# Optimization experiments

Measured on AMD Instinct MI355X. Metric: run time of the kernel, lower is better.

## Reference

```python
import jax, jax.numpy as jnp
import numpy as np

B, C, H, W = 8, 256, 128, 128
HEADS = 8


def setup_inputs() -> dict:
    key = jax.random.key(0)
    ks = jax.random.split(key, 9)
    d = {"x": jax.random.normal(ks[0], (B, C, H, W), jnp.float32)}
    for i, name in enumerate(["q", "k", "v", "o"]):
        # 1x1 conv == dense over channel dim; weight [C_out, C_in]
        d["W" + name] = jax.random.normal(ks[1 + 2 * i], (C, C), jnp.float32) * (C ** -0.5)
        d["b" + name] = jax.random.normal(ks[2 + 2 * i], (C,), jnp.float32) * 0.01
    return d


def reference(x, Wq, bq, Wk, bk, Wv, bv, Wo, bo):
    b, c, h, w = x.shape
    heads = HEADS
    hd = c // heads
    scale = hd ** -0.5

    def proj(Wm, bm):
        y = jnp.einsum('bchw,oc->bohw', x, Wm) + bm[None, :, None, None]
        return y.reshape(b, heads, hd, h, w)

    q = proj(Wq, bq)
    k = proj(Wk, bk)
    v = proj(Wv, bv)

    # horizontal attention: per row y, attention over width positions (w x v)
    attn_h = jax.nn.softmax(jnp.einsum('bhdyw,bhdyv->bhywv', q, k) * scale, axis=-1)
    out_h = jnp.einsum('bhywv,bhdyv->bhdyw', attn_h, v)

    # vertical attention: per column w, attention over height positions (y x z)
    attn_w = jax.nn.softmax(jnp.einsum('bhdyw,bhdzw->bhwyz', q, k) * scale, axis=-1)
    out_w = jnp.einsum('bhwyz,bhdzw->bhdyw', attn_w, v)

    out = (out_h + out_w).reshape(b, c, h, w)
    out = jnp.einsum('bchw,oc->bohw', out, Wo) + bo[None, :, None, None]
    return out + x
```

## Files before the change

### kernel.cpp

```cpp
#include <hip/hip_runtime.h>

#define B_ 8
#define C_ 256
#define HH 128
#define WW 128
#define HEADS_ 8
#define SCALE 0.17677669529663687f

typedef short v8s __attribute__((ext_vector_type(8)));
typedef float f32x4 __attribute__((ext_vector_type(4)));

__device__ __forceinline__ unsigned short f2bf(float f){
  unsigned int u = __float_as_uint(f);
  u += 0x7FFFu + ((u>>16)&1u);
  return (unsigned short)(u>>16);
}
__device__ __forceinline__ float bf2f(unsigned short s){ return __uint_as_float(((unsigned int)s)<<16); }
__device__ __forceinline__ f32x4 mfma16(v8s a, v8s b, f32x4 c){
  return __builtin_amdgcn_mfma_f32_16x16x32_bf16(a,b,c,0,0,0);
}
__device__ __forceinline__ int xs_idx(int s,int c){ return s*256 + ((((c>>3)^(s&31))&31)<<3) + (c&7); }
__device__ __forceinline__ int wl_idx(int dm,int c){ return dm*256 + ((((c>>3)^(dm&31))&31)<<3) + (c&7); }
__device__ __forceinline__ void gload_lds16(const void* g, void* l){
  __builtin_amdgcn_global_load_lds((const __attribute__((address_space(1))) unsigned int*)g,
                                   (__attribute__((address_space(3))) unsigned int*)l, 16, 0, 0);
}

#define WS_NEED1 201850880ULL
#define WS_NEED2 268959744ULL

__global__ __launch_bounds__(512,4)
void prep_w_kernel(const float* __restrict__ Wq, const float* __restrict__ Wk,
                   const float* __restrict__ Wv, const float* __restrict__ Wo,
                   unsigned short* __restrict__ wsW, unsigned short* __restrict__ wsWo){
  const int bid = blockIdx.x, t = threadIdx.x;
  if (bid < 96){
    int h = bid/12, seg = bid%12;
    int dm = seg*8 + (t>>6), c = (t&63)*4;
    const float* Wm = dm<32 ? Wq : (dm<64 ? Wk : Wv);
    const float4 w4 = *(const float4*)&Wm[(h*32 + (dm&31))*C_ + c];
    ushort4 pk = { f2bf(w4.x), f2bf(w4.y), f2bf(w4.z), f2bf(w4.w) };
    *(ushort4*)(wsW + h*24576 + wl_idx(dm, c)) = pk;
  } else {
    int q = bid - 96;
    int oc = q>>2, seg = q&3;
    int o = seg*8 + (t>>6), c = (t&63)*4;
    const float4 w4 = *(const float4*)&Wo[(oc*32+o)*C_ + c];
    ushort4 pk = { f2bf(w4.x), f2bf(w4.y), f2bf(w4.z), f2bf(w4.w) };
    *(ushort4*)(wsWo + oc*8192 + wl_idx(o, c)) = pk;
  }
}

__global__ __launch_bounds__(512,2)
void proj_kernel(const float* __restrict__ x,
                 const float* __restrict__ bq, const float* __restrict__ bk,
                 const float* __restrict__ bv,
                 const unsigned short* __restrict__ wsW,
                 unsigned short* __restrict__ Qw, unsigned short* __restrict__ Kw,
                 unsigned short* __restrict__ Vw){
  __shared__ __align__(16) char smem[141696];
  unsigned short* xs = (unsigned short*)smem;
  unsigned short* wl = (unsigned short*)(smem + 65536);
  unsigned short* rp = (unsigned short*)(smem + 114688);
  float* biasl       = (float*)(smem + 141312);

  const int tid = threadIdx.x;
  const int b = blockIdx.x >> 7, pt = blockIdx.x & 127;
  const size_t pos0 = (size_t)pt * 128;

  {
    const int cq = (tid>>5)*2, pl = (tid&31)*4;
    #pragma unroll
    for (int j=0;j<8;++j){
      int c0 = j*32 + cq;
      const float4 a0 = *(const float4*)&x[((size_t)(b*C_ + c0  ))*16384 + pos0 + pl];
      const float4 a1 = *(const float4*)&x[((size_t)(b*C_ + c0+1))*16384 + pos0 + pl];
      unsigned int p0 = (unsigned)f2bf(a0.x) | ((unsigned)f2bf(a1.x)<<16);
      unsigned int p1 = (unsigned)f2bf(a0.y) | ((unsigned)f2bf(a1.y)<<16);
      unsigned int p2 = (unsigned)f2bf(a0.z) | ((unsigned)f2bf(a1.z)<<16);
      unsigned int p3 = (unsigned)f2bf(a0.w) | ((unsigned)f2bf(a1.w)<<16);
      *(unsigned int*)&xs[xs_idx(pl+0, c0)] = p0;
      *(unsigned int*)&xs[xs_idx(pl+1, c0)] = p1;
      *(unsigned int*)&xs[xs_idx(pl+2, c0)] = p2;
      *(unsigned int*)&xs[xs_idx(pl+3, c0)] = p3;
    }
  }
  {
    const char* wb = (const char*)wsW;
    for (int rIt=0;rIt<6;++rIt)
      gload_lds16(wb + (rIt*512+tid)*16, (char*)wl + (rIt*512+tid)*16);
  }

  const int lane = tid&63, wv = tid>>6, lr = lane&15, lk = lane>>4;
  const f32x4 zero4 = {0.f,0.f,0.f,0.f};

  for (int h=0; h<HEADS_; ++h){
    __syncthreads();
    if (tid<96){
      int mat = tid>>5;
      const float* bm = mat==0?bq:(mat==1?bk:bv);
      biasl[tid] = bm[h*32 + (tid&31)];
    }
    f32x4 acc[6];
    #pragma unroll
    for (int n=0;n<6;++n) acc[n]=zero4;
    #pragma unroll
    for (int ks=0;ks<8;++ks){
      int c0 = ks*32 + lk*8;
      v8s a = *(const v8s*)(xs + xs_idx(wv*16+lr, c0));
      #pragma unroll
      for (int n=0;n<6;++n){
        v8s bb = *(const v8s*)(wl + wl_idx(n*16+lr, c0));
        acc[n] = mfma16(a, bb, acc[n]);
      }
    }
    __syncthreads();
    if (h < HEADS_-1){
      const char* wb = (const char*)wsW + (h+1)*49152;
      for (int rIt=0;rIt<6;++rIt)
        gload_lds16(wb + (rIt*512+tid)*16, (char*)wl + (rIt*512+tid)*16);
    }
    #pragma unroll
    for (int n=0;n<6;++n){
      int dm = n*16+lr;
      float bia = biasl[dm];
      #pragma unroll
      for (int rr=0;rr<4;++rr){
        int pos = wv*16 + lk*4 + rr;
        float val = acc[n][rr] + bia;
        if (n<2) val *= SCALE;
        rp[pos*104 + dm] = f2bf(val);
      }
    }
    __syncthreads();
    {
      int pos = tid>>2, ch = tid&3;
      v8s qd = *(const v8s*)&rp[pos*104 +      ch*8];
      v8s kd = *(const v8s*)&rp[pos*104 + 32 + ch*8];
      v8s vd = *(const v8s*)&rp[pos*104 + 64 + ch*8];
      size_t ob = ((size_t)(b*HEADS_+h)*16384 + pos0 + pos)*32 + ch*8;
      *(v8s*)(Qw + ob) = qd;
      *(v8s*)(Kw + ob) = kd;
      *(v8s*)(Vw + ob) = vd;
    }
  }
}

template<int VERT>
__global__ __launch_bounds__(512,6)
void attn2_kernel(const unsigned short* __restrict__ Qw, const unsigned short* __restrict__ Kw,
                  const unsigned short* __restrict__ Vw, unsigned short* __restrict__ Ah){
  __shared__ __align__(16) char smem[37376];
  unsigned short* kl = (unsigned short*)smem;
  unsigned short* Vt = (unsigned short*)(smem + 10240);
  float*          ob = (float*)(smem + 18944);

  const int tid = threadIdx.x;
  int b, head, fix;
  if (VERT){ int xcd = blockIdx.x&7, rest = blockIdx.x>>3;
             fix = xcd*16 + (rest&15); head = (rest>>4)&7; b = rest>>7; }
  else     { head = blockIdx.x&7; fix = (blockIdx.x>>3)&127; b = blockIdx.x>>10; }
  const size_t tb = (size_t)(b*HEADS_+head)*16384*32;
  const int lane = tid&63, wvq = tid>>6, lr = lane&15, lk = lane>>4;
  const f32x4 zero4 = {0.f,0.f,0.f,0.f};

  {
    int pl = tid>>2, ch = tid&3;
    size_t g = tb + (VERT ? ((size_t)pl*128 + fix) : ((size_t)fix*128 + pl))*32 + ch*8;
    v8s kv = *(const v8s*)(Kw + g);
    v8s vv = *(const v8s*)(Vw + g);
    *(v8s*)&kl[pl*40 + ch*8] = kv;
    int slot = (pl & ~31) | (((pl>>2)&3)<<3) | (((pl>>4)&1)<<2) | (pl&3);
    #pragma unroll
    for (int j=0;j<8;++j) Vt[(ch*8+j)*136 + slot] = (unsigned short)vv[j];
  }
  const int posq = VERT ? (wvq*16+lr)*128 + fix : fix*128 + (wvq*16+lr);
  v8s qa = *(const v8s*)(Qw + tb + (size_t)posq*32 + lk*8);
  __syncthreads();

  f32x4 sc[8];
  #pragma unroll
  for (int kt=0;kt<8;++kt){
    v8s kb = *(const v8s*)&kl[(kt*16+lr)*40 + lk*8];
    sc[kt] = mfma16(kb, qa, zero4);
  }
  float mx = sc[0][0];
  #pragma unroll
  for (int kt=0;kt<8;++kt){
    #pragma unroll
    for (int rr=0;rr<4;++rr) mx = fmaxf(mx, sc[kt][rr]);
  }
  mx = fmaxf(mx, __shfl_xor(mx, 16));
  mx = fmaxf(mx, __shfl_xor(mx, 32));
  float sm = 0.f;
  #pragma unroll
  for (int kt=0;kt<8;++kt){
    #pragma unroll
    for (int rr=0;rr<4;++rr){ float p = __expf(sc[kt][rr]-mx); sc[kt][rr]=p; sm += p; }
  }
  sm += __shfl_xor(sm, 16);
  sm += __shfl_xor(sm, 32);
  const float rn = 1.f/sm;
  unsigned int pk[16];
  #pragma unroll
  for (int kt=0;kt<8;++kt){
    pk[kt*2  ] = (unsigned)f2bf(sc[kt][0]*rn) | ((unsigned)f2bf(sc[kt][1]*rn)<<16);
    pk[kt*2+1] = (unsigned)f2bf(sc[kt][2]*rn) | ((unsigned)f2bf(sc[kt][3]*rn)<<16);
  }
  f32x4 o0 = zero4, o1 = zero4;
  #pragma unroll
  for (int ks=0;ks<4;++ks){
    union { unsigned int u[4]; v8s v; } pa;
    pa.u[0]=pk[4*ks]; pa.u[1]=pk[4*ks+1]; pa.u[2]=pk[4*ks+2]; pa.u[3]=pk[4*ks+3];
    v8s v0 = *(const v8s*)&Vt[(     lr)*136 + ks*32 + lk*8];
    v8s v1 = *(const v8s*)&Vt[(16 + lr)*136 + ks*32 + lk*8];
    o0 = mfma16(pa.v, v0, o0);
    o1 = mfma16(pa.v, v1, o1);
  }
  #pragma unroll
  for (int rr=0;rr<4;++rr){
    int s = wvq*16 + lk*4 + rr;
    ob[s*36 + lr     ] = o0[rr];
    ob[s*36 + 16 + lr] = o1[rr];
  }
  {
    int row = wvq*16 + (lane>>2), jj = lane&3;
    f32x4 fa = *(const f32x4*)&ob[row*36 + jj*8];
    f32x4 fb = *(const f32x4*)&ob[row*36 + jj*8 + 4];
    int pos = VERT ? row*128 + fix : fix*128 + row;
    size_t ga = ((size_t)b*16384 + pos)*256 + (size_t)(((head*4+jj)^(pos&31))<<3);
    if (VERT){
      v8s prev = *(const v8s*)(Ah + ga);
      v8s outv;
      #pragma unroll
      for (int j=0;j<4;++j){
        outv[j]   = (short)f2bf(bf2f((unsigned short)prev[j])   + fa[j]);
        outv[4+j] = (short)f2bf(bf2f((unsigned short)prev[4+j]) + fb[j]);
      }
      *(v8s*)(Ah + ga) = outv;
    } else {
      v8s outv;
      #pragma unroll
      for (int j=0;j<4;++j){
        outv[j]   = (short)f2bf(fa[j]);
        outv[4+j] = (short)f2bf(fb[j]);
      }
      *(v8s*)(Ah + ga) = outv;
    }
  }
}

__global__ __launch_bounds__(512,1)
void final2_kernel(const float* __restrict__ x, const unsigned short* __restrict__ wsWo,
                   const float* __restrict__ bo, const unsigned short* __restrict__ Ah,
                   float* __restrict__ out)
{
  __shared__ __align__(16) char smem[82048];
  unsigned short* asl = (unsigned short*)smem;
  unsigned short* wol = (unsigned short*)(smem + 65536);
  float* bol          = (float*)(smem + 81920);

  const int tid = threadIdx.x;
  const int b = blockIdx.x >> 7, pt = blockIdx.x & 127;
  {
    const char* ab = (const char*)(Ah + ((size_t)b*16384 + (size_t)pt*128)*256);
    for (int i=0;i<8;++i)
      gload_lds16(ab + (i*512+tid)*16, (char*)asl + (i*512+tid)*16);
  }
  const int lane = tid & 63, wv = tid >> 6;
  const int lr = lane & 15, lk = lane >> 4;
  const f32x4 zero4 = {0.f,0.f,0.f,0.f};

  for (int oc = 0; oc < 8; ++oc){
    {
      const char* wb = (const char*)wsWo + oc*16384;
      for (int rIt=0;rIt<2;++rIt)
        gload_lds16(wb + (rIt*512+tid)*16, (char*)wol + (rIt*512+tid)*16);
    }
    if (tid < 32) bol[tid] = bo[oc*32 + tid];
    __syncthreads();

    f32x4 a0 = zero4, a1 = zero4;
    #pragma unroll
    for (int ks = 0; ks < 8; ++ks){
      int c0 = ks*32 + lk*8;
      v8s av = *(const v8s*)(asl + xs_idx(wv*16 + lr, c0));
      v8s b0 = *(const v8s*)(wol + wl_idx(     lr, c0));
      v8s b1 = *(const v8s*)(wol + wl_idx(16 + lr, c0));
      a0 = mfma16(av, b0, a0);
      a1 = mfma16(av, b1, a1);
    }
    {
      int base0 = ((b*C_ + oc*32 + lr)*HH)*WW + pt*128 + wv*16 + lk*4;
      f32x4 xv0 = *(const f32x4*)(x + base0);
      f32x4 xv1 = *(const f32x4*)(x + base0 + 16*HH*WW);
      f32x4 r0 = a0 + xv0 + bol[lr];
      f32x4 r1 = a1 + xv1 + bol[16 + lr];
      *(f32x4*)(out + base0) = r0;
      *(f32x4*)(out + base0 + 16*HH*WW) = r1;
    }
    __syncthreads();
  }
}

template<int VERT>
__global__ __launch_bounds__(512,4)
void attn_kernel(const unsigned short* __restrict__ Qw, const unsigned short* __restrict__ Kw,
                 const unsigned short* __restrict__ Vw, float* __restrict__ osum){
  __shared__ __align__(16) char smem[53760];
  unsigned short* kl = (unsigned short*)smem;
  unsigned short* Vt = (unsigned short*)(smem + 10240);
  unsigned short* Pl = (unsigned short*)(smem + 18944);

  const int tid = threadIdx.x;
  int b, head, fix;
  if (VERT){ int xcd = blockIdx.x&7, rest = blockIdx.x>>3;
             fix = xcd*16 + (rest&15); head = (rest>>4)&7; b = rest>>7; }
  else     { head = blockIdx.x&7; fix = (blockIdx.x>>3)&127; b = blockIdx.x>>10; }
  const size_t tb = (size_t)(b*HEADS_+head)*16384*32;
  const int lane = tid&63, wv = tid>>6, lr = lane&15, lk = lane>>4;

  {
    int pl = tid>>2, ch = tid&3;
    size_t g = tb + ( VERT ? ((size_t)pl*128 + fix) : ((size_t)fix*128 + pl) )*32 + ch*8;
    v8s kv = *(const v8s*)(Kw + g);
    v8s vv = *(const v8s*)(Vw + g);
    *(v8s*)&kl[pl*40 + ch*8] = kv;
    #pragma unroll
    for (int j=0;j<8;++j) Vt[(ch*8+j)*136 + pl] = (unsigned short)vv[j];
  }
  const int posq = VERT ? (wv*16+lr)*128 + fix : fix*128 + wv*16+lr;
  v8s qa = *(const v8s*)(Qw + tb + (size_t)posq*32 + lk*8);
  __syncthreads();

  const f32x4 zero4 = {0.f,0.f,0.f,0.f};
  f32x4 sc[8];
  #pragma unroll
  for (int kt=0;kt<8;++kt){
    v8s kb = *(const v8s*)&kl[(kt*16+lr)*40 + lk*8];
    sc[kt] = mfma16(qa, kb, zero4);
  }
  float rn[4];
  #pragma unroll
  for (int rr=0;rr<4;++rr){
    float mx = sc[0][rr];
    #pragma unroll
    for (int kt=1;kt<8;++kt) mx = fmaxf(mx, sc[kt][rr]);
    #pragma unroll
    for (int off=1;off<16;off<<=1) mx = fmaxf(mx, __shfl_xor(mx, off, 16));
    float sm = 0.f;
    const int prow = (wv*16 + lk*4 + rr)*136;
    #pragma unroll
    for (int kt=0;kt<8;++kt){
      float p = __expf(sc[kt][rr]-mx);
      sm += p;
      Pl[prow + kt*16 + lr] = f2bf(p);
    }
    #pragma unroll
    for (int off=1;off<16;off<<=1) sm += __shfl_xor(sm, off, 16);
    rn[rr] = 1.f/sm;
  }
  f32x4 o0 = zero4, o1 = zero4;
  #pragma unroll
  for (int ks=0;ks<4;++ks){
    v8s pa = *(const v8s*)&Pl[(wv*16+lr)*136 + ks*32 + lk*8];
    v8s v0 = *(const v8s*)&Vt[(     lr)*136 + ks*32 + lk*8];
    v8s v1 = *(const v8s*)&Vt[(16 + lr)*136 + ks*32 + lk*8];
    o0 = mfma16(pa, v0, o0);
    o1 = mfma16(pa, v1, o1);
  }
  f32x4 rnv = {rn[0],rn[1],rn[2],rn[3]};
  o0 *= rnv; o1 *= rnv;
  if (!VERT){
    size_t base = ((size_t)(b*C_ + head*32 + lr)*HH + fix)*WW + wv*16 + lk*4;
    *(f32x4*)(osum + base) = o0;
    *(f32x4*)(osum + base + (size_t)16*HH*WW) = o1;
  } else {
    #pragma unroll
    for (int rr=0;rr<4;++rr){
      size_t g = ((size_t)(b*C_ + head*32 + lr)*HH + wv*16+lk*4+rr)*WW + fix;
      osum[g] += o0[rr];
      osum[g + (size_t)16*HH*WW] += o1[rr];
    }
  }
}

__global__ __launch_bounds__(512,1)
void final_fast_kernel(const float* __restrict__ x, const unsigned short* __restrict__ wsWo,
                       const float* __restrict__ bo, float* __restrict__ out)
{
  __shared__ __align__(16) char smem[82048];
  unsigned short* asl = (unsigned short*)smem;
  unsigned short* wol = (unsigned short*)(smem + 65536);
  float* bol          = (float*)(smem + 81920);

  const int tid = threadIdx.x;
  const int b = blockIdx.x >> 7, r = blockIdx.x & 127;
  {
    const int w = tid & 127, part = tid >> 7;
    #pragma unroll 4
    for (int it = 0; it < 32; ++it){
      int c = (it*4 + part)*2;
      int g0 = ((b*C_ + c)*HH + r)*WW + w;
      float f0 = out[g0], f1 = out[g0 + HH*WW];
      unsigned int pkv = (unsigned int)f2bf(f0) | ((unsigned int)f2bf(f1)<<16);
      *(unsigned int*)(asl + xs_idx(w,c)) = pkv;
    }
  }
  const int lane = tid & 63, wv = tid >> 6;
  const int lr = lane & 15, lk = lane >> 4;
  const f32x4 zero4 = {0.f,0.f,0.f,0.f};

  for (int oc = 0; oc < 8; ++oc){
    {
      const char* wb = (const char*)wsWo + oc*16384;
      for (int rIt=0;rIt<2;++rIt)
        gload_lds16(wb + (rIt*512+tid)*16, (char*)wol + (rIt*512+tid)*16);
    }
    if (tid < 32) bol[tid] = bo[oc*32 + tid];
    __syncthreads();

    f32x4 a0 = zero4, a1 = zero4;
    #pragma unroll
    for (int ks = 0; ks < 8; ++ks){
      int c0 = ks*32 + lk*8;
      v8s av = *(const v8s*)(asl + xs_idx(wv*16 + lr, c0));
      v8s b0 = *(const v8s*)(wol + wl_idx(     lr, c0));
      v8s b1 = *(const v8s*)(wol + wl_idx(16 + lr, c0));
      a0 = mfma16(av, b0, a0);
      a1 = mfma16(av, b1, a1);
    }
    {
      int base0 = ((b*C_ + oc*32 + lr)*HH + r)*WW + wv*16 + lk*4;
      f32x4 xv0 = *(const f32x4*)(x + base0);
      f32x4 xv1 = *(const f32x4*)(x + base0 + 16*HH*WW);
      f32x4 r0 = a0 + xv0 + bol[lr];
      f32x4 r1 = a1 + xv1 + bol[16 + lr];
      *(f32x4*)(out + base0) = r0;
      *(f32x4*)(out + base0 + 16*HH*WW) = r1;
    }
    __syncthreads();
  }
}

extern "C" void kernel_launch(void* const* d_in, const int* in_sizes, int n_in,
                              void* d_out, int out_size, void* d_ws, size_t ws_size,
                              hipStream_t stream) {
  const float* x  = (const float*)d_in[0];
  const float* Wq = (const float*)d_in[1];
  const float* bq = (const float*)d_in[2];
  const float* Wk = (const float*)d_in[3];
  const float* bk = (const float*)d_in[4];
  const float* Wv = (const float*)d_in[5];
  const float* bv = (const float*)d_in[6];
  const float* Wo = (const float*)d_in[7];
  const float* bo = (const float*)d_in[8];
  float* out = (float*)d_out;

  unsigned short* wsW  = (unsigned short*)d_ws;
  unsigned short* wsWo = (unsigned short*)((char*)d_ws + 393216);
  unsigned short* Qw   = (unsigned short*)((char*)d_ws + 524288);
  unsigned short* Kw   = Qw + 33554432;
  unsigned short* Vw   = Kw + 33554432;
  unsigned short* Ah   = (unsigned short*)((char*)d_ws + WS_NEED1);

  prep_w_kernel<<<dim3(128),  dim3(512), 0, stream>>>(Wq, Wk, Wv, Wo, wsW, wsWo);
  proj_kernel  <<<dim3(1024), dim3(512), 0, stream>>>(x, bq, bk, bv, wsW, Qw, Kw, Vw);
  if (ws_size >= WS_NEED2) {
    attn2_kernel<0><<<dim3(8192), dim3(512), 0, stream>>>(Qw, Kw, Vw, Ah);
    attn2_kernel<1><<<dim3(8192), dim3(512), 0, stream>>>(Qw, Kw, Vw, Ah);
    final2_kernel<<<dim3(1024), dim3(512), 0, stream>>>(x, wsWo, bo, Ah, out);
  } else {
    attn_kernel<0><<<dim3(8192), dim3(512), 0, stream>>>(Qw, Kw, Vw, out);
    attn_kernel<1><<<dim3(8192), dim3(512), 0, stream>>>(Qw, Kw, Vw, out);
    final_fast_kernel<<<dim3(1024), dim3(512), 0, stream>>>(x, wsWo, bo, out);
  }
}
```

Baseline: 313.6 us.

## Fuse horizontal attention into projection kernel and drop fallback path

The projection kernel now computes horizontal (row) attention directly from the Q/K/V tile it already holds in LDS for each row, and writes the head output into the Ah buffer. This removes the separate horizontal attention launch and its re-read of Q/K/V from global memory. The fallback path for small workspaces is removed, so the workspace-size check is gone. The larger LDS footprint lowers occupancy to one block per CU and adds serial attention work inside the projection loop.

```diff
diff --git a/kernel.cpp b/kernel.cpp
--- a/kernel.cpp
+++ b/kernel.cpp
@@ -26,8 +26,7 @@
                                    (__attribute__((address_space(3))) unsigned int*)l, 16, 0, 0);
 }
 
-#define WS_NEED1 201850880ULL
-#define WS_NEED2 268959744ULL
+#define WS_OFF_AH 201850880ULL
 
 __global__ __launch_bounds__(512,4)
 void prep_w_kernel(const float* __restrict__ Wq, const float* __restrict__ Wk,
@@ -51,22 +50,24 @@
   }
 }
 
-__global__ __launch_bounds__(512,2)
-void proj_kernel(const float* __restrict__ x,
-                 const float* __restrict__ bq, const float* __restrict__ bk,
-                 const float* __restrict__ bv,
-                 const unsigned short* __restrict__ wsW,
-                 unsigned short* __restrict__ Qw, unsigned short* __restrict__ Kw,
-                 unsigned short* __restrict__ Vw){
-  __shared__ __align__(16) char smem[141696];
+__global__ __launch_bounds__(512,1)
+void projh_kernel(const float* __restrict__ x,
+                  const float* __restrict__ bq, const float* __restrict__ bk,
+                  const float* __restrict__ bv,
+                  const unsigned short* __restrict__ wsW,
+                  unsigned short* __restrict__ Qw, unsigned short* __restrict__ Kw,
+                  unsigned short* __restrict__ Vw, unsigned short* __restrict__ Ah){
+  __shared__ __align__(16) char smem[150400];
   unsigned short* xs = (unsigned short*)smem;
   unsigned short* wl = (unsigned short*)(smem + 65536);
   unsigned short* rp = (unsigned short*)(smem + 114688);
-  float* biasl       = (float*)(smem + 141312);
+  float*          ob = (float*)(smem + 114688);
+  unsigned short* Vt = (unsigned short*)(smem + 141312);
+  float* biasl       = (float*)(smem + 150016);
 
   const int tid = threadIdx.x;
-  const int b = blockIdx.x >> 7, pt = blockIdx.x & 127;
-  const size_t pos0 = (size_t)pt * 128;
+  const int b = blockIdx.x >> 7, y = blockIdx.x & 127;
+  const size_t pos0 = (size_t)y * 128;
 
   {
     const int cq = (tid>>5)*2, pl = (tid&31)*4;
@@ -129,19 +130,85 @@
         int pos = wv*16 + lk*4 + rr;
         float val = acc[n][rr] + bia;
         if (n<2) val *= SCALE;
-        rp[pos*104 + dm] = f2bf(val);
+        unsigned short bv16 = f2bf(val);
+        rp[pos*104 + dm] = bv16;
+        if (n>=4){
+          int slot = (pos & ~31) | (((pos>>2)&3)<<3) | (((pos>>4)&1)<<2) | (pos&3);
+          Vt[((n-4)*16+lr)*136 + slot] = bv16;
+        }
       }
     }
     __syncthreads();
     {
-      int pos = tid>>2, ch = tid&3;
-      v8s qd = *(const v8s*)&rp[pos*104 +      ch*8];
-      v8s kd = *(const v8s*)&rp[pos*104 + 32 + ch*8];
-      v8s vd = *(const v8s*)&rp[pos*104 + 64 + ch*8];
-      size_t ob = ((size_t)(b*HEADS_+h)*16384 + pos0 + pos)*32 + ch*8;
-      *(v8s*)(Qw + ob) = qd;
-      *(v8s*)(Kw + ob) = kd;
-      *(v8s*)(Vw + ob) = vd;
+      int p = tid>>2, ch = tid&3;
+      v8s qd = *(const v8s*)&rp[p*104 +      ch*8];
+      v8s kd = *(const v8s*)&rp[p*104 + 32 + ch*8];
+      v8s vd = *(const v8s*)&rp[p*104 + 64 + ch*8];
+      size_t og = ((size_t)(b*HEADS_+h)*16384 + pos0 + p)*32 + ch*8;
+      *(v8s*)(Qw + og) = qd;
+      *(v8s*)(Kw + og) = kd;
+      *(v8s*)(Vw + og) = vd;
+    }
+    v8s qa = *(const v8s*)&rp[(wv*16+lr)*104 + lk*8];
+    f32x4 sc[8];
+    #pragma unroll
+    for (int kt=0;kt<8;++kt){
+      v8s kb = *(const v8s*)&rp[(kt*16+lr)*104 + 32 + lk*8];
+      sc[kt] = mfma16(kb, qa, zero4);
+    }
+    float mx = sc[0][0];
+    #pragma unroll
+    for (int kt=0;kt<8;++kt){
+      #pragma unroll
+      for (int rr=0;rr<4;++rr) mx = fmaxf(mx, sc[kt][rr]);
+    }
+    mx = fmaxf(mx, __shfl_xor(mx, 16));
+    mx = fmaxf(mx, __shfl_xor(mx, 32));
+    float sm = 0.f;
+    #pragma unroll
+    for (int kt=0;kt<8;++kt){
+      #pragma unroll
+      for (int rr=0;rr<4;++rr){ float p = __expf(sc[kt][rr]-mx); sc[kt][rr]=p; sm += p; }
+    }
+    sm += __shfl_xor(sm, 16);
+    sm += __shfl_xor(sm, 32);
+    const float rn = 1.f/sm;
+    unsigned int pk[16];
+    #pragma unroll
+    for (int kt=0;kt<8;++kt){
+      pk[kt*2  ] = (unsigned)f2bf(sc[kt][0]*rn) | ((unsigned)f2bf(sc[kt][1]*rn)<<16);
+      pk[kt*2+1] = (unsigned)f2bf(sc[kt][2]*rn) | ((unsigned)f2bf(sc[kt][3]*rn)<<16);
+    }
+    f32x4 o0 = zero4, o1 = zero4;
+    #pragma unroll
+    for (int ks=0;ks<4;++ks){
+      union { unsigned int u[4]; v8s v; } pa;
+      pa.u[0]=pk[4*ks]; pa.u[1]=pk[4*ks+1]; pa.u[2]=pk[4*ks+2]; pa.u[3]=pk[4*ks+3];
+      v8s v0 = *(const v8s*)&Vt[(     lr)*136 + ks*32 + lk*8];
+      v8s v1 = *(const v8s*)&Vt[(16 + lr)*136 + ks*32 + lk*8];
+      o0 = mfma16(pa.v, v0, o0);
+      o1 = mfma16(pa.v, v1, o1);
+    }
+    __syncthreads();
+    #pragma unroll
+    for (int rr=0;rr<4;++rr){
+      int s = wv*16 + lk*4 + rr;
+      ob[s*36 + lr     ] = o0[rr];
+      ob[s*36 + 16 + lr] = o1[rr];
+    }
+    {
+      int row = wv*16 + (lane>>2), jj = lane&3;
+      f32x4 fa = *(const f32x4*)&ob[row*36 + jj*8];
+      f32x4 fb = *(const f32x4*)&ob[row*36 + jj*8 + 4];
+      int pos = y*128 + row;
+      size_t ga = ((size_t)b*16384 + pos)*256 + (size_t)(((h*4+jj)^(pos&31))<<3);
+      v8s outv;
+      #pragma unroll
+      for (int j=0;j<4;++j){
+        outv[j]   = (short)f2bf(fa[j]);
+        outv[4+j] = (short)f2bf(fb[j]);
+      }
+      *(v8s*)(Ah + ga) = outv;
     }
   }
 }
@@ -292,146 +359,6 @@
     }
     {
       int base0 = ((b*C_ + oc*32 + lr)*HH)*WW + pt*128 + wv*16 + lk*4;
-      f32x4 xv0 = *(const f32x4*)(x + base0);
-      f32x4 xv1 = *(const f32x4*)(x + base0 + 16*HH*WW);
-      f32x4 r0 = a0 + xv0 + bol[lr];
-      f32x4 r1 = a1 + xv1 + bol[16 + lr];
-      *(f32x4*)(out + base0) = r0;
-      *(f32x4*)(out + base0 + 16*HH*WW) = r1;
-    }
-    __syncthreads();
-  }
-}
-
-template<int VERT>
-__global__ __launch_bounds__(512,4)
-void attn_kernel(const unsigned short* __restrict__ Qw, const unsigned short* __restrict__ Kw,
-                 const unsigned short* __restrict__ Vw, float* __restrict__ osum){
-  __shared__ __align__(16) char smem[53760];
-  unsigned short* kl = (unsigned short*)smem;
-  unsigned short* Vt = (unsigned short*)(smem + 10240);
-  unsigned short* Pl = (unsigned short*)(smem + 18944);
-
-  const int tid = threadIdx.x;
-  int b, head, fix;
-  if (VERT){ int xcd = blockIdx.x&7, rest = blockIdx.x>>3;
-             fix = xcd*16 + (rest&15); head = (rest>>4)&7; b = rest>>7; }
-  else     { head = blockIdx.x&7; fix = (blockIdx.x>>3)&127; b = blockIdx.x>>10; }
-  const size_t tb = (size_t)(b*HEADS_+head)*16384*32;
-  const int lane = tid&63, wv = tid>>6, lr = lane&15, lk = lane>>4;
-
-  {
-    int pl = tid>>2, ch = tid&3;
-    size_t g = tb + ( VERT ? ((size_t)pl*128 + fix) : ((size_t)fix*128 + pl) )*32 + ch*8;
-    v8s kv = *(const v8s*)(Kw + g);
-    v8s vv = *(const v8s*)(Vw + g);
-    *(v8s*)&kl[pl*40 + ch*8] = kv;
-    #pragma unroll
-    for (int j=0;j<8;++j) Vt[(ch*8+j)*136 + pl] = (unsigned short)vv[j];
-  }
-  const int posq = VERT ? (wv*16+lr)*128 + fix : fix*128 + wv*16+lr;
-  v8s qa = *(const v8s*)(Qw + tb + (size_t)posq*32 + lk*8);
-  __syncthreads();
-
-  const f32x4 zero4 = {0.f,0.f,0.f,0.f};
-  f32x4 sc[8];
-  #pragma unroll
-  for (int kt=0;kt<8;++kt){
-    v8s kb = *(const v8s*)&kl[(kt*16+lr)*40 + lk*8];
-    sc[kt] = mfma16(qa, kb, zero4);
-  }
-  float rn[4];
-  #pragma unroll
-  for (int rr=0;rr<4;++rr){
-    float mx = sc[0][rr];
-    #pragma unroll
-    for (int kt=1;kt<8;++kt) mx = fmaxf(mx, sc[kt][rr]);
-    #pragma unroll
-    for (int off=1;off<16;off<<=1) mx = fmaxf(mx, __shfl_xor(mx, off, 16));
-    float sm = 0.f;
-    const int prow = (wv*16 + lk*4 + rr)*136;
-    #pragma unroll
-    for (int kt=0;kt<8;++kt){
-      float p = __expf(sc[kt][rr]-mx);
-      sm += p;
-      Pl[prow + kt*16 + lr] = f2bf(p);
-    }
-    #pragma unroll
-    for (int off=1;off<16;off<<=1) sm += __shfl_xor(sm, off, 16);
-    rn[rr] = 1.f/sm;
-  }
-  f32x4 o0 = zero4, o1 = zero4;
-  #pragma unroll
-  for (int ks=0;ks<4;++ks){
-    v8s pa = *(const v8s*)&Pl[(wv*16+lr)*136 + ks*32 + lk*8];
-    v8s v0 = *(const v8s*)&Vt[(     lr)*136 + ks*32 + lk*8];
-    v8s v1 = *(const v8s*)&Vt[(16 + lr)*136 + ks*32 + lk*8];
-    o0 = mfma16(pa, v0, o0);
-    o1 = mfma16(pa, v1, o1);
-  }
-  f32x4 rnv = {rn[0],rn[1],rn[2],rn[3]};
-  o0 *= rnv; o1 *= rnv;
-  if (!VERT){
-    size_t base = ((size_t)(b*C_ + head*32 + lr)*HH + fix)*WW + wv*16 + lk*4;
-    *(f32x4*)(osum + base) = o0;
-    *(f32x4*)(osum + base + (size_t)16*HH*WW) = o1;
-  } else {
-    #pragma unroll
-    for (int rr=0;rr<4;++rr){
-      size_t g = ((size_t)(b*C_ + head*32 + lr)*HH + wv*16+lk*4+rr)*WW + fix;
-      osum[g] += o0[rr];
-      osum[g + (size_t)16*HH*WW] += o1[rr];
-    }
-  }
-}
-
-__global__ __launch_bounds__(512,1)
-void final_fast_kernel(const float* __restrict__ x, const unsigned short* __restrict__ wsWo,
-                       const float* __restrict__ bo, float* __restrict__ out)
-{
-  __shared__ __align__(16) char smem[82048];
-  unsigned short* asl = (unsigned short*)smem;
-  unsigned short* wol = (unsigned short*)(smem + 65536);
-  float* bol          = (float*)(smem + 81920);
-
-  const int tid = threadIdx.x;
-  const int b = blockIdx.x >> 7, r = blockIdx.x & 127;
-  {
-    const int w = tid & 127, part = tid >> 7;
-    #pragma unroll 4
-    for (int it = 0; it < 32; ++it){
-      int c = (it*4 + part)*2;
-      int g0 = ((b*C_ + c)*HH + r)*WW + w;
-      float f0 = out[g0], f1 = out[g0 + HH*WW];
-      unsigned int pkv = (unsigned int)f2bf(f0) | ((unsigned int)f2bf(f1)<<16);
-      *(unsigned int*)(asl + xs_idx(w,c)) = pkv;
-    }
-  }
-  const int lane = tid & 63, wv = tid >> 6;
-  const int lr = lane & 15, lk = lane >> 4;
-  const f32x4 zero4 = {0.f,0.f,0.f,0.f};
-
-  for (int oc = 0; oc < 8; ++oc){
-    {
-      const char* wb = (const char*)wsWo + oc*16384;
-      for (int rIt=0;rIt<2;++rIt)
-        gload_lds16(wb + (rIt*512+tid)*16, (char*)wol + (rIt*512+tid)*16);
-    }
-    if (tid < 32) bol[tid] = bo[oc*32 + tid];
-    __syncthreads();
-
-    f32x4 a0 = zero4, a1 = zero4;
-    #pragma unroll
-    for (int ks = 0; ks < 8; ++ks){
-      int c0 = ks*32 + lk*8;
-      v8s av = *(const v8s*)(asl + xs_idx(wv*16 + lr, c0));
-      v8s b0 = *(const v8s*)(wol + wl_idx(     lr, c0));
-      v8s b1 = *(const v8s*)(wol + wl_idx(16 + lr, c0));
-      a0 = mfma16(av, b0, a0);
-      a1 = mfma16(av, b1, a1);
-    }
-    {
-      int base0 = ((b*C_ + oc*32 + lr)*HH + r)*WW + wv*16 + lk*4;
       f32x4 xv0 = *(const f32x4*)(x + base0);
       f32x4 xv1 = *(const f32x4*)(x + base0 + 16*HH*WW);
       f32x4 r0 = a0 + xv0 + bol[lr];
@@ -462,17 +389,10 @@
   unsigned short* Qw   = (unsigned short*)((char*)d_ws + 524288);
   unsigned short* Kw   = Qw + 33554432;
   unsigned short* Vw   = Kw + 33554432;
-  unsigned short* Ah   = (unsigned short*)((char*)d_ws + WS_NEED1);
+  unsigned short* Ah   = (unsigned short*)((char*)d_ws + WS_OFF_AH);
 
   prep_w_kernel<<<dim3(128),  dim3(512), 0, stream>>>(Wq, Wk, Wv, Wo, wsW, wsWo);
-  proj_kernel  <<<dim3(1024), dim3(512), 0, stream>>>(x, bq, bk, bv, wsW, Qw, Kw, Vw);
-  if (ws_size >= WS_NEED2) {
-    attn2_kernel<0><<<dim3(8192), dim3(512), 0, stream>>>(Qw, Kw, Vw, Ah);
-    attn2_kernel<1><<<dim3(8192), dim3(512), 0, stream>>>(Qw, Kw, Vw, Ah);
-    final2_kernel<<<dim3(1024), dim3(512), 0, stream>>>(x, wsWo, bo, Ah, out);
-  } else {
-    attn_kernel<0><<<dim3(8192), dim3(512), 0, stream>>>(Qw, Kw, Vw, out);
-    attn_kernel<1><<<dim3(8192), dim3(512), 0, stream>>>(Qw, Kw, Vw, out);
-    final_fast_kernel<<<dim3(1024), dim3(512), 0, stream>>>(x, wsWo, bo, out);
-  }
-}
+  projh_kernel <<<dim3(1024), dim3(512), 0, stream>>>(x, bq, bk, bv, wsW, Qw, Kw, Vw, Ah);
+  attn2_kernel<1><<<dim3(8192), dim3(512), 0, stream>>>(Qw, Kw, Vw, Ah);
+  final2_kernel<<<dim3(1024), dim3(512), 0, stream>>>(x, wsWo, bo, Ah, out);
+}
```

Result: slower. 335.8 us (+7.1%).
